# Kernel tuning notes

Hardware: AMD Instinct MI355X
Metric: run time of the kernel (lower is better)

## Reference

```python
import jax, jax.numpy as jnp
import numpy as np

NUM_TOKENS_SCORE = 64
NUM_HEADS = 16
NUM_KV_HEADS = 4
HEAD_SIZE = 128
SCALE = 0.08838834764831845  # 1/sqrt(128)


def setup_inputs() -> dict:
    key = jax.random.key(0)
    k1, k2, k3 = jax.random.split(key, 3)
    B, S = 2, 2048
    total = B * S
    return {
        "query": jax.random.normal(k1, (total, NUM_HEADS * HEAD_SIZE), dtype=jnp.float32),
        "key": jax.random.normal(k2, (total, NUM_KV_HEADS * HEAD_SIZE), dtype=jnp.float32),
        "value": jax.random.normal(k3, (total, NUM_KV_HEADS * HEAD_SIZE), dtype=jnp.float32),
        "batch_size": B,
        "seq_len": S,
    }


def reference(query, key, value, batch_size, seq_len):
    """Prompt-phase SparsePagedAttention: varlen causal GQA attention (equal
    prompt lengths -> dense [B,S] layout) plus the fused softmax score-sum over
    the last NUM_TOKENS_SCORE query rows used for KV-cache pruning."""
    B, S = batch_size, seq_len
    H, Hk, D = NUM_HEADS, NUM_KV_HEADS, HEAD_SIZE
    rep = H // Hk  # queries per kv head (head_mapping via repeat_interleave)

    q = query.reshape(B, S, H, D)
    k = jnp.repeat(key.reshape(B, S, Hk, D), rep, axis=2)    # [B,S,H,D]
    v = jnp.repeat(value.reshape(B, S, Hk, D), rep, axis=2)  # [B,S,H,D]

    scores = jnp.einsum('bqhd,bkhd->bhqk', q, k) * SCALE      # [B,H,S,S]
    causal = jnp.tril(jnp.ones((S, S), dtype=bool))
    scores = jnp.where(causal[None, None], scores, jnp.finfo(scores.dtype).min)
    probs = jax.nn.softmax(scores, axis=-1)                   # [B,H,S,S]

    out = jnp.einsum('bhqk,bkhd->bqhd', probs, v).reshape(B * S, H * D)
    # triton_fused_softmax_sum: sum softmax probs over last NUM_TOKENS_SCORE queries
    score_sum = probs[:, :, S - NUM_TOKENS_SCORE:, :].sum(axis=2)  # [B,H,S]
    return out, score_sum
```

## Files before the change

kernel.cpp:

```cpp
#include <hip/hip_runtime.h>


#define BB 2
#define SS 2048
#define NH 16
#define NKV 4
#define DD 128
#define TILE_SH 4096

typedef __attribute__((ext_vector_type(8))) short bf16x8;
typedef __attribute__((ext_vector_type(4))) float f32x4;

constexpr float SCL = 0.08838834764831845f * 1.4426950408889634f;

__device__ __forceinline__ short f2bf(float f) {
  union { float f; unsigned u; } v; v.f = f;
  unsigned r = v.u + 0x7FFFu + ((v.u >> 16) & 1u);
  return (short)(r >> 16);
}

__device__ __forceinline__ unsigned pack2bf(float a, float b) {
  union { float f; unsigned u; } x, y; x.f = a; y.f = b;
  return __builtin_amdgcn_perm(y.u, x.u, 0x07060302);
}

__device__ __forceinline__ void gl_lds16(const void* g, void* l) {
  __builtin_amdgcn_global_load_lds(
      (const __attribute__((address_space(1))) unsigned*)g,
      (__attribute__((address_space(3))) unsigned*)l, 16, 0, 0);
}

__global__ void prep(const float* __restrict__ K, const float* __restrict__ V,
                     short* __restrict__ Kb, short* __restrict__ Vb) {
  const int p = blockIdx.x;
  const int b = p >> 8, hk = (p >> 6) & 3, kt = p & 63;
  const int tid = threadIdx.x;
  const int k0 = kt * 32;
  short* kb = Kb + ((size_t)((b * 4 + hk) * 64 + kt)) * TILE_SH;
  short* vb = Vb + ((size_t)((b * 4 + hk) * 64 + kt)) * TILE_SH;
  {
    const int k = tid & 31, chb = tid >> 5;
    const float* src = K + ((size_t)(b * SS + k0 + k) * NKV + hk) * DD;
#pragma unroll
    for (int i = 0; i < 2; ++i) {
      const int ch = chb + i * 8;
      const float* s = src + ch * 8;
      float4 f0 = *(const float4*)s;
      float4 f1 = *(const float4*)(s + 4);
      bf16x8 t;
      t[0] = f2bf(f0.x); t[1] = f2bf(f0.y); t[2] = f2bf(f0.z); t[3] = f2bf(f0.w);
      t[4] = f2bf(f1.x); t[5] = f2bf(f1.y); t[6] = f2bf(f1.z); t[7] = f2bf(f1.w);
      *(bf16x8*)(kb + (ch * 32 + k) * 8) = t;
    }
  }
  {
    const int d = tid & 127, kcb = tid >> 7;
#pragma unroll
    for (int i = 0; i < 2; ++i) {
      const int kc = kcb + i * 2;
      const float* s = V + ((size_t)(b * SS + k0 + kc * 8) * NKV + hk) * DD + d;
      bf16x8 t;
#pragma unroll
      for (int e = 0; e < 8; ++e) t[e] = f2bf(s[(size_t)e * (NKV * DD)]);
      *(bf16x8*)(vb + (kc * 128 + d) * 8) = t;
    }
  }
}

__global__ __launch_bounds__(256, 4) void fa2(
    const float* __restrict__ Q, const short* __restrict__ Kb,
    const short* __restrict__ Vb, float* __restrict__ Out,
    float* __restrict__ wsl) {
  __shared__ bf16x8 kv[2][1024];
  __shared__ short ldsP[4][640];

  const int tid = threadIdx.x;
  const int w = tid >> 6, lane = tid & 63;
  const int c = lane & 15, qd = lane >> 4;

  const int i = blockIdx.x;
  const int g = i >> 8, cc = i & 255;
  const int bh = cc >> 3, jp = cc & 7;
  const int qt = (g == 0) ? jp : (g == 1) ? 31 - jp : (g == 2) ? 8 + jp : 23 - jp;
  const int b = bh >> 4, h = bh & 15, hk = h >> 2;

  const char* KT = (const char*)(Kb + ((size_t)(b * 4 + hk)) * 64 * TILE_SH);
  const char* VT = (const char*)(Vb + ((size_t)(b * 4 + hk)) * 64 * TILE_SH);

  auto stage = [&](int iv, int bi) {
    const char* sk = KT + (size_t)iv * 16384 + w * 4096 + lane * 16;
    char* dk = (char*)kv[bi] + w * 4096;
#pragma unroll
    for (int t = 0; t < 4; ++t) gl_lds16(sk + t * 1024, dk + t * 1024);
  };

  stage(0, 0);

  const float* qrow = Q + ((size_t)(b * SS + qt * 64 + w * 16 + c) * NH + h) * DD;
  bf16x8 qf[4];
#pragma unroll
  for (int ks = 0; ks < 4; ++ks) {
    const float* p = qrow + ks * 32 + qd * 8;
    float4 f0 = *(const float4*)p;
    float4 f1 = *(const float4*)(p + 4);
    bf16x8 tq;
    tq[0] = f2bf(f0.x * SCL); tq[1] = f2bf(f0.y * SCL);
    tq[2] = f2bf(f0.z * SCL); tq[3] = f2bf(f0.w * SCL);
    tq[4] = f2bf(f1.x * SCL); tq[5] = f2bf(f1.y * SCL);
    tq[6] = f2bf(f1.z * SCL); tq[7] = f2bf(f1.w * SCL);
    qf[ks] = tq;
  }

  f32x4 o[8];
#pragma unroll
  for (int dt = 0; dt < 8; ++dt) { o[dt][0] = 0.f; o[dt][1] = 0.f; o[dt][2] = 0.f; o[dt][3] = 0.f; }
  float l_part = 0.f;

  const int niv = qt + 1;

  auto qkp = [&](const bf16x8* bKt, int kt) -> bf16x8 {
    f32x4 st0 = {0.f, 0.f, 0.f, 0.f}, st1 = {0.f, 0.f, 0.f, 0.f};
#pragma unroll
    for (int ks = 0; ks < 4; ++ks) {
      const int chz = (ks * 4 + qd) * 32;
      bf16x8 a0 = bKt[chz + c];
      bf16x8 a1 = bKt[chz + 16 + c];
      st0 = __builtin_amdgcn_mfma_f32_16x16x32_bf16(a0, qf[ks], st0, 0, 0, 0);
      st1 = __builtin_amdgcn_mfma_f32_16x16x32_bf16(a1, qf[ks], st1, 0, 0, 0);
    }
    float pr[8];
#pragma unroll
    for (int r = 0; r < 4; ++r) { pr[r] = exp2f(st0[r]); pr[4 + r] = exp2f(st1[r]); }
    const int koff = kt * 32 - qt * 64;
    if (koff >= 0) {
      const int qrl = w * 16 + c;
#pragma unroll
      for (int mt = 0; mt < 2; ++mt)
#pragma unroll
        for (int r = 0; r < 4; ++r)
          if (koff + mt * 16 + qd * 4 + r > qrl) pr[mt * 4 + r] = 0.f;
    }
#pragma unroll
    for (int x = 0; x < 8; ++x) l_part += pr[x];

    short* pp = ldsP[w] + c * 40;
#pragma unroll
    for (int mt = 0; mt < 2; ++mt) {
      union { short4 s4; unsigned u[2]; } pk;
      pk.u[0] = pack2bf(pr[mt * 4 + 0], pr[mt * 4 + 1]);
      pk.u[1] = pack2bf(pr[mt * 4 + 2], pr[mt * 4 + 3]);
      *(short4*)(pp + mt * 16 + qd * 4) = pk.s4;
    }
    __asm__ volatile("s_waitcnt lgkmcnt(0)" ::: "memory");
    return *(const bf16x8*)(pp + qd * 8);
  };

  for (int iv = 0; iv < niv; ++iv) {
    __syncthreads();
    const int cb = iv & 1;
    const bf16x8* bK = kv[cb];

    bf16x8 av0[8];
    const bf16x8* vg0 =
        (const bf16x8*)(VT + (size_t)(2 * iv) * 8192) + (qd * 128 + c);
#pragma unroll
    for (int dt = 0; dt < 8; ++dt) av0[dt] = vg0[dt * 16];

    bf16x8 pf0 = qkp(bK, 2 * iv);

#pragma unroll
    for (int dt = 0; dt < 8; ++dt)
      o[dt] = __builtin_amdgcn_mfma_f32_16x16x32_bf16(av0[dt], pf0, o[dt], 0, 0, 0);

    bf16x8 av1[8];
    const bf16x8* vg1 =
        (const bf16x8*)(VT + (size_t)(2 * iv + 1) * 8192) + (qd * 128 + c);
#pragma unroll
    for (int dt = 0; dt < 8; ++dt) av1[dt] = vg1[dt * 16];

    if (iv + 1 < niv) stage(iv + 1, cb ^ 1);

    bf16x8 pf1 = qkp(bK + 512, 2 * iv + 1);

#pragma unroll
    for (int dt = 0; dt < 8; ++dt)
      o[dt] = __builtin_amdgcn_mfma_f32_16x16x32_bf16(av1[dt], pf1, o[dt], 0, 0, 0);
  }

  float l = l_part;
  l += __shfl_xor(l, 16);
  l += __shfl_xor(l, 32);
  const float linv = 1.f / l;

  float* orow = Out + ((size_t)(b * SS + qt * 64 + w * 16 + c) * NH + h) * DD;
#pragma unroll
  for (int dt = 0; dt < 8; ++dt) {
    float4 ov;
    ov.x = o[dt][0] * linv; ov.y = o[dt][1] * linv;
    ov.z = o[dt][2] * linv; ov.w = o[dt][3] * linv;
    *(float4*)(orow + dt * 16 + qd * 4) = ov;
  }
  if (qt == 31 && qd == 0)
    wsl[bh * 64 + w * 16 + c] = l;
}

__global__ __launch_bounds__(256, 2) void score(
    const float* __restrict__ Q, const short* __restrict__ Kb,
    const float* __restrict__ wsl, float* __restrict__ out2) {
  __shared__ float ldsS[4][64];
  const int tid = threadIdx.x;
  const int w = tid >> 6, lane = tid & 63;
  const int c = lane & 15, qd = lane >> 4;
  const int bh = blockIdx.x & 31, kt = blockIdx.x >> 5;
  const int b = bh >> 4, h = bh & 15, hk = h >> 2;
  const int q0 = SS - 64;

  const float* qrow = Q + ((size_t)(b * SS + q0 + w * 16 + c) * NH + h) * DD;
  bf16x8 qf[4];
#pragma unroll
  for (int ks = 0; ks < 4; ++ks) {
    const float* p = qrow + ks * 32 + qd * 8;
    float4 f0 = *(const float4*)p;
    float4 f1 = *(const float4*)(p + 4);
    bf16x8 t;
    t[0] = f2bf(f0.x * SCL); t[1] = f2bf(f0.y * SCL);
    t[2] = f2bf(f0.z * SCL); t[3] = f2bf(f0.w * SCL);
    t[4] = f2bf(f1.x * SCL); t[5] = f2bf(f1.y * SCL);
    t[6] = f2bf(f1.z * SCL); t[7] = f2bf(f1.w * SCL);
    qf[ks] = t;
  }
  float linv[4];
  const int r0 = bh * 64 + w * 16 + qd * 4;
#pragma unroll
  for (int r = 0; r < 4; ++r) linv[r] = 1.f / wsl[r0 + r];

  const bf16x8* kb = (const bf16x8*)Kb + ((size_t)(b * 4 + hk) * 64 + kt * 2) * 512;
  f32x4 s[4];
#pragma unroll
  for (int nt = 0; nt < 4; ++nt) { s[nt][0] = 0.f; s[nt][1] = 0.f; s[nt][2] = 0.f; s[nt][3] = 0.f; }
#pragma unroll
  for (int ks = 0; ks < 4; ++ks) {
#pragma unroll
    for (int nt = 0; nt < 4; ++nt) {
      bf16x8 kf = kb[(nt >> 1) * 512 + (ks * 4 + qd) * 32 + (nt & 1) * 16 + c];
      s[nt] = __builtin_amdgcn_mfma_f32_16x16x32_bf16(qf[ks], kf, s[nt], 0, 0, 0);
    }
  }
  const bool diag = (kt == 31);
  float cs[4] = {0.f, 0.f, 0.f, 0.f};
#pragma unroll
  for (int nt = 0; nt < 4; ++nt) {
#pragma unroll
    for (int r = 0; r < 4; ++r) {
      float pv = exp2f(s[nt][r]) * linv[r];
      if (diag && nt * 16 + c > w * 16 + qd * 4 + r) pv = 0.f;
      cs[nt] += pv;
    }
    cs[nt] += __shfl_xor(cs[nt], 16);
    cs[nt] += __shfl_xor(cs[nt], 32);
  }
  if (lane < 16) {
#pragma unroll
    for (int nt = 0; nt < 4; ++nt) ldsS[w][nt * 16 + c] = cs[nt];
  }
  __syncthreads();
  if (tid < 64)
    out2[(size_t)bh * SS + kt * 64 + tid] =
        ldsS[0][tid] + ldsS[1][tid] + ldsS[2][tid] + ldsS[3][tid];
}

extern "C" void kernel_launch(void* const* d_in, const int* in_sizes, int n_in,
                              void* d_out, int out_size, void* d_ws, size_t ws_size,
                              hipStream_t stream) {
  const float* Q = (const float*)d_in[0];
  const float* K = (const float*)d_in[1];
  const float* V = (const float*)d_in[2];
  float* out = (float*)d_out;
  float* out2 = out + (size_t)BB * SS * NH * DD;

  short* Kb = (short*)d_ws;
  const size_t tsz = (size_t)2 * 4 * 64 * TILE_SH;
  short* Vb = Kb + tsz;
  float* wsl = (float*)(Vb + tsz);

  hipLaunchKernelGGL(prep, dim3(512), dim3(256), 0, stream, K, V, Kb, Vb);
  hipLaunchKernelGGL(fa2, dim3(1024), dim3(256), 0, stream, Q, Kb, Vb, out, wsl);
  hipLaunchKernelGGL(score, dim3(1024), dim3(256), 0, stream, Q, Kb, wsl, out2);
}
```

Measured before the change: 159.3 us.

## Permute V key layout so P fragments stay in registers, drop LDS round trip

The V pre-conversion kernel now interleaves keys within each 8-element chunk (keys e&3 + 16*(e>>2)). This makes the QK MFMA output layout match the B-operand layout needed by the PV MFMA, so the P tile is packed to bf16 directly in registers instead of being written to and read back from per-wave LDS. The QK accumulation is also split into two independent accumulator chains to shorten MFMA dependency latency. This removes LDS traffic and a waitcnt stall, at the cost of a few extra adds and registers.

```diff
diff --git a/kernel.cpp b/kernel.cpp
--- a/kernel.cpp
+++ b/kernel.cpp
@@ -58,10 +58,11 @@
 #pragma unroll
     for (int i = 0; i < 2; ++i) {
       const int kc = kcb + i * 2;
-      const float* s = V + ((size_t)(b * SS + k0 + kc * 8) * NKV + hk) * DD + d;
+      const float* s = V + ((size_t)(b * SS + k0 + kc * 4) * NKV + hk) * DD + d;
       bf16x8 t;
 #pragma unroll
-      for (int e = 0; e < 8; ++e) t[e] = f2bf(s[(size_t)e * (NKV * DD)]);
+      for (int e = 0; e < 8; ++e)
+        t[e] = f2bf(s[(size_t)((e & 3) + 16 * (e >> 2)) * (NKV * DD)]);
       *(bf16x8*)(vb + (kc * 128 + d) * 8) = t;
     }
   }
@@ -72,7 +73,6 @@
     const short* __restrict__ Vb, float* __restrict__ Out,
     float* __restrict__ wsl) {
   __shared__ bf16x8 kv[2][1024];
-  __shared__ short ldsP[4][640];
 
   const int tid = threadIdx.x;
   const int w = tid >> 6, lane = tid & 63;
@@ -119,18 +119,30 @@
   const int niv = qt + 1;
 
   auto qkp = [&](const bf16x8* bKt, int kt) -> bf16x8 {
-    f32x4 st0 = {0.f, 0.f, 0.f, 0.f}, st1 = {0.f, 0.f, 0.f, 0.f};
-#pragma unroll
-    for (int ks = 0; ks < 4; ++ks) {
+    f32x4 s0a = {0.f, 0.f, 0.f, 0.f}, s0b = {0.f, 0.f, 0.f, 0.f};
+    f32x4 s1a = {0.f, 0.f, 0.f, 0.f}, s1b = {0.f, 0.f, 0.f, 0.f};
+#pragma unroll
+    for (int ks = 0; ks < 2; ++ks) {
       const int chz = (ks * 4 + qd) * 32;
       bf16x8 a0 = bKt[chz + c];
       bf16x8 a1 = bKt[chz + 16 + c];
-      st0 = __builtin_amdgcn_mfma_f32_16x16x32_bf16(a0, qf[ks], st0, 0, 0, 0);
-      st1 = __builtin_amdgcn_mfma_f32_16x16x32_bf16(a1, qf[ks], st1, 0, 0, 0);
+      s0a = __builtin_amdgcn_mfma_f32_16x16x32_bf16(a0, qf[ks], s0a, 0, 0, 0);
+      s1a = __builtin_amdgcn_mfma_f32_16x16x32_bf16(a1, qf[ks], s1a, 0, 0, 0);
+    }
+#pragma unroll
+    for (int ks = 2; ks < 4; ++ks) {
+      const int chz = (ks * 4 + qd) * 32;
+      bf16x8 a0 = bKt[chz + c];
+      bf16x8 a1 = bKt[chz + 16 + c];
+      s0b = __builtin_amdgcn_mfma_f32_16x16x32_bf16(a0, qf[ks], s0b, 0, 0, 0);
+      s1b = __builtin_amdgcn_mfma_f32_16x16x32_bf16(a1, qf[ks], s1b, 0, 0, 0);
     }
     float pr[8];
 #pragma unroll
-    for (int r = 0; r < 4; ++r) { pr[r] = exp2f(st0[r]); pr[4 + r] = exp2f(st1[r]); }
+    for (int r = 0; r < 4; ++r) {
+      pr[r] = exp2f(s0a[r] + s0b[r]);
+      pr[4 + r] = exp2f(s1a[r] + s1b[r]);
+    }
     const int koff = kt * 32 - qt * 64;
     if (koff >= 0) {
       const int qrl = w * 16 + c;
@@ -143,16 +155,12 @@
 #pragma unroll
     for (int x = 0; x < 8; ++x) l_part += pr[x];
 
-    short* pp = ldsP[w] + c * 40;
-#pragma unroll
-    for (int mt = 0; mt < 2; ++mt) {
-      union { short4 s4; unsigned u[2]; } pk;
-      pk.u[0] = pack2bf(pr[mt * 4 + 0], pr[mt * 4 + 1]);
-      pk.u[1] = pack2bf(pr[mt * 4 + 2], pr[mt * 4 + 3]);
-      *(short4*)(pp + mt * 16 + qd * 4) = pk.s4;
-    }
-    __asm__ volatile("s_waitcnt lgkmcnt(0)" ::: "memory");
-    return *(const bf16x8*)(pp + qd * 8);
+    union { unsigned u[4]; bf16x8 v; } pk;
+    pk.u[0] = pack2bf(pr[0], pr[1]);
+    pk.u[1] = pack2bf(pr[2], pr[3]);
+    pk.u[2] = pack2bf(pr[4], pr[5]);
+    pk.u[3] = pack2bf(pr[6], pr[7]);
+    return pk.v;
   };
 
   for (int iv = 0; iv < niv; ++iv) {
```

After: 192.0 us. 1.2x slower.
